# Optimization experiments

Measured on AMD Instinct MI355X. Metric: run time of the kernel, lower is better.

## Reference

```python
import jax, jax.numpy as jnp
import numpy as np

H = 4  # heads


def _tconv(x, src, dst, ea, Wq, bq, Wk, bk, Wv, bv, We, Ws, bs):
    # PyG TransformerConv, heads=4, concat=False, root_weight=True, beta=False
    N = x.shape[0]
    Dh = Wq.shape[1] // H  # per-head dim (= hidden_channels)
    q = (x @ Wq + bq).reshape(N, H, Dh)
    k = (x @ Wk + bk).reshape(N, H, Dh)
    v = (x @ Wv + bv).reshape(N, H, Dh)
    e = (ea @ We).reshape(-1, H, Dh)      # lin_edge has no bias in PyG
    kj = k[src] + e                        # [E, H, Dh]
    vj = v[src] + e                        # [E, H, Dh]
    alpha = (q[dst] * kj).sum(-1) / jnp.sqrt(jnp.asarray(Dh, x.dtype))  # [E, H]
    # segment softmax over incoming edges of each dst node
    m = jax.ops.segment_max(alpha, dst, num_segments=N)
    a = jnp.exp(alpha - m[dst])
    s = jax.ops.segment_sum(a, dst, num_segments=N)
    a = a / (s[dst] + 1e-16)
    out = jax.ops.segment_sum(a[:, :, None] * vj, dst, num_segments=N)  # [N, H, Dh]
    out = out.mean(axis=1)                 # concat=False -> mean over heads
    return out + x @ Ws + bs               # root/skip connection


def setup_inputs() -> dict:
    key = jax.random.key(0)
    ks = jax.random.split(key, 32)
    N, E, C_in, C_e, Ch = 50000, 800000, 32, 16, 32
    d = {}
    d['x'] = jax.random.normal(ks[0], (N, C_in), dtype=jnp.float32)
    d['edge_attr'] = jax.random.normal(ks[1], (E, C_e), dtype=jnp.float32)
    d['edge_index'] = jax.random.randint(ks[2], (2, E), 0, N, dtype=jnp.int32)
    s = 0.05
    i = 3
    for L, cin in ((1, C_in), (2, Ch)):
        d[f'Wq{L}'] = jax.random.normal(ks[i], (cin, H * Ch)) * s; i += 1
        d[f'bq{L}'] = jnp.zeros((H * Ch,), jnp.float32)
        d[f'Wk{L}'] = jax.random.normal(ks[i], (cin, H * Ch)) * s; i += 1
        d[f'bk{L}'] = jnp.zeros((H * Ch,), jnp.float32)
        d[f'Wv{L}'] = jax.random.normal(ks[i], (cin, H * Ch)) * s; i += 1
        d[f'bv{L}'] = jnp.zeros((H * Ch,), jnp.float32)
        d[f'We{L}'] = jax.random.normal(ks[i], (C_e, H * Ch)) * s; i += 1
        d[f'Ws{L}'] = jax.random.normal(ks[i], (cin, Ch)) * s; i += 1
        d[f'bs{L}'] = jnp.zeros((Ch,), jnp.float32)
    d['Wm1'] = jax.random.normal(ks[i], (2 * Ch + C_e, Ch)) * s; i += 1
    d['bm1'] = jnp.zeros((Ch,), jnp.float32)
    d['Wm2'] = jax.random.normal(ks[i], (Ch, 1)) * s; i += 1
    d['bm2'] = jnp.zeros((1,), jnp.float32)
    return d


def reference(x, edge_attr, edge_index,
              Wq1, bq1, Wk1, bk1, Wv1, bv1, We1, Ws1, bs1,
              Wq2, bq2, Wk2, bk2, Wv2, bv2, We2, Ws2, bs2,
              Wm1, bm1, Wm2, bm2):
    src, dst = edge_index[0], edge_index[1]
    h = jax.nn.relu(_tconv(x, src, dst, edge_attr, Wq1, bq1, Wk1, bk1, Wv1, bv1, We1, Ws1, bs1))
    h = jax.nn.relu(_tconv(h, src, dst, edge_attr, Wq2, bq2, Wk2, bk2, Wv2, bv2, We2, Ws2, bs2))
    ef = jnp.concatenate([h[src], edge_attr, h[dst]], axis=-1)  # [E, 2*Ch + C_e]
    out = jax.nn.relu(ef @ Wm1 + bm1) @ Wm2 + bm2
    return out.reshape(-1)
```

## Files before the change

kernel.cpp:

```cpp
#include <hip/hip_runtime.h>
#include <hip/hip_fp16.h>
#include <math.h>

#define D128 128
#define CH32 32
#define CE16 16

__global__ void k_hist(const int* __restrict__ dst, int* __restrict__ deg, int E) {
    int e = blockIdx.x * blockDim.x + threadIdx.x;
    if (e < E) atomicAdd(&deg[dst[e]], 1);
}

__global__ void k_scan1(const int* __restrict__ deg, int* __restrict__ offs,
                        int* __restrict__ bsum, int N) {
    __shared__ int buf[256];
    int t = threadIdx.x;
    int i = blockIdx.x * 256 + t;
    int v = (i < N) ? deg[i] : 0;
    buf[t] = v;
    __syncthreads();
    #pragma unroll
    for (int off = 1; off < 256; off <<= 1) {
        int val = (t >= off) ? buf[t - off] : 0;
        __syncthreads();
        buf[t] += val;
        __syncthreads();
    }
    if (i < N) offs[i] = buf[t] - v;
    if (t == 255) bsum[blockIdx.x] = buf[255];
}

__global__ void k_scan2(const int* __restrict__ bsum, int* __restrict__ boff, int nb) {
    __shared__ int buf[256];
    int t = threadIdx.x;
    int v = (t < nb) ? bsum[t] : 0;
    buf[t] = v;
    __syncthreads();
    #pragma unroll
    for (int off = 1; off < 256; off <<= 1) {
        int val = (t >= off) ? buf[t - off] : 0;
        __syncthreads();
        buf[t] += val;
        __syncthreads();
    }
    if (t < nb) boff[t] = buf[t] - v;
}

__global__ void k_scan3(const int* __restrict__ boff, int* __restrict__ offs,
                        int* __restrict__ cur, int N, int E) {
    int i = blockIdx.x * blockDim.x + threadIdx.x;
    if (i < N) {
        int o = offs[i] + boff[i >> 8];
        offs[i] = o;
        cur[i] = o;
    }
    if (i == 0) offs[N] = E;
}

__global__ void k_scatter(const int* __restrict__ src, const int* __restrict__ dst,
                          int* __restrict__ cur, int* __restrict__ csr_srcb,
                          float4* __restrict__ ea_csr4, const float4* __restrict__ ea4,
                          int E) {
    int e = blockIdx.x * blockDim.x + threadIdx.x;
    if (e < E) {
        int d = dst[e];
        int p = atomicAdd(&cur[d], 1);
        csr_srcb[p] = src[e] << 9;
        float4 a0 = ea4[e * 4 + 0];
        float4 a1 = ea4[e * 4 + 1];
        float4 a2 = ea4[e * 4 + 2];
        float4 a3 = ea4[e * 4 + 3];
        ea_csr4[p * 4 + 0] = a0;
        ea_csr4[p * 4 + 1] = a1;
        ea_csr4[p * 4 + 2] = a2;
        ea_csr4[p * 4 + 3] = a3;
    }
}

__global__ void k_wqe(const float* __restrict__ Wq, const float* __restrict__ bq,
                      const float* __restrict__ We,
                      float* __restrict__ Wqe, float* __restrict__ bqe) {
    int t = threadIdx.x;
    int h = t >> 4, j = t & 15;
    const float QS = 0.17677669529663687f * 1.4426950408889634f;
    float wecol[32];
    #pragma unroll
    for (int d = 0; d < 32; d++) wecol[d] = We[j * D128 + h * 32 + d];
    for (int i = 0; i < 32; i++) {
        float s = 0.f;
        #pragma unroll
        for (int d = 0; d < 32; d++) s = fmaf(Wq[i * D128 + h * 32 + d], wecol[d], s);
        Wqe[i * 64 + t] = s * QS;
    }
    float s = 0.f;
    #pragma unroll
    for (int d = 0; d < 32; d++) s = fmaf(bq[h * 32 + d], wecol[d], s);
    bqe[t] = s * QS;
}

__global__ __launch_bounds__(256) void k_qeproj(
    const float* __restrict__ x, const float* __restrict__ Wqe,
    const float* __restrict__ bqe, float* __restrict__ qeb, int N) {
    __shared__ float W[32][64];
    __shared__ float xs[4][32];
    int tid = threadIdx.x;
    for (int i = tid; i < 32 * 64; i += 256) W[i >> 6][i & 63] = Wqe[i];
    int col = tid & 63, r = tid >> 6;
    float b = bqe[col];
    __syncthreads();
    int nchunk = (N + 3) / 4;
    for (int chk = blockIdx.x; chk < nchunk; chk += gridDim.x) {
        int n = chk * 4 + r;
        if (tid < 128) {
            int rr = tid >> 5, cc = tid & 31;
            int nn = chk * 4 + rr;
            xs[rr][cc] = (nn < N) ? x[nn * 32 + cc] : 0.f;
        }
        __syncthreads();
        if (n < N) {
            float a = b;
            #pragma unroll
            for (int j = 0; j < 32; j++) a = fmaf(xs[r][j], W[j][col], a);
            qeb[(size_t)n * 64 + col] = a;
        }
        __syncthreads();
    }
}

__global__ __launch_bounds__(128) void k_nodeproj(
    const float* __restrict__ xin,
    const float* __restrict__ Wq, const float* __restrict__ bq,
    const float* __restrict__ Wk, const float* __restrict__ bk,
    const float* __restrict__ Wv, const float* __restrict__ bv,
    const float* __restrict__ Ws, const float* __restrict__ bs,
    float* __restrict__ q, __half* __restrict__ kvh,
    float* __restrict__ skip, int N)
{
    int tid = threadIdx.x;
    int c   = tid & 31;
    int pos = ((tid >> 2) << 3) | (tid & 3);
    float wq[32], wk[32], wv[32], ws[32];
    #pragma unroll
    for (int j = 0; j < 32; j++) {
        wq[j] = Wq[j * D128 + tid];
        wk[j] = Wk[j * D128 + tid];
        wv[j] = Wv[j * D128 + tid];
        ws[j] = Ws[j * CH32 + c];
    }
    float bqc = bq[tid], bkc = bk[tid], bvc = bv[tid], bsc = bs[c];
    __shared__ float xs[4][32];
    int nchunk = (N + 3) / 4;
    for (int chk = blockIdx.x; chk < nchunk; chk += gridDim.x) {
        int base = chk * 4;
        {
            int r = tid >> 5;
            int n = base + r;
            xs[r][c] = (n < N) ? xin[n * 32 + c] : 0.f;
        }
        __syncthreads();
        #pragma unroll
        for (int r = 0; r < 4; r++) {
            int n = base + r;
            if (n < N) {
                float aq = bqc, ak = bkc, av = bvc;
                #pragma unroll
                for (int j = 0; j < 32; j++) {
                    float xj = xs[r][j];
                    aq = fmaf(xj, wq[j], aq);
                    ak = fmaf(xj, wk[j], ak);
                    av = fmaf(xj, wv[j], av);
                }
                q[n * D128 + tid] = aq;
                kvh[(size_t)n * 256 + pos]     = __float2half_rn(ak);
                kvh[(size_t)n * 256 + pos + 4] = __float2half_rn(av);
            }
        }
        {
            int r = tid >> 5;
            int n = base + r;
            if (n < N) {
                float as = bsc;
                #pragma unroll
                for (int j = 0; j < 32; j++) as = fmaf(xs[r][j], ws[j], as);
                skip[n * 32 + c] = as;
            }
        }
        __syncthreads();
    }
}

__global__ __launch_bounds__(64) void k_edgeattn(
    const float* __restrict__ q, const __half* __restrict__ kvh,
    const float* __restrict__ skip,
    const float* __restrict__ ea_csr, const float* __restrict__ We,
    const int* __restrict__ offs, const int* __restrict__ csr_srcb,
    const float* __restrict__ qeb, float* __restrict__ hout)
{
    int node = blockIdx.x;
    int lane = threadIdx.x;
    int eg   = lane >> 5;
    int c    = lane & 31;
    int g    = c & 7;
    int c4   = c << 2;

    const float QS = 0.17677669529663687f * 1.4426950408889634f;
    float4 qv = *(const float4*)&q[(size_t)node * D128 + c4];
    qv.x *= QS; qv.y *= QS; qv.z *= QS; qv.w *= QS;

    float2 qe01 = *(const float2*)&qeb[(size_t)node * 64 + ((c >> 3) << 4) + 2 * g];
    float qe0 = qe01.x, qe1 = qe01.y;

    int s0 = offs[node], s1 = offs[node + 1];
    int deg = s1 - s0;

    float l = 0.f;
    float ac0 = 0.f, ac1 = 0.f, ac2 = 0.f, ac3 = 0.f;
    float se0 = 0.f, se1 = 0.f;

    if (deg > 0) {
        int last = s1 - 1;
        const char* kvb = (const char*)kvh;
        int toff = c << 4;

        auto eidx = [&](int p) { return min(s0 + 2 * p + eg, last); };
        auto ldidx = [&](int p) { return csr_srcb[eidx(p)]; };
        auto ldkv  = [&](int ib) {
            return *(const float4*)(kvb + (size_t)(unsigned)ib + toff);
        };
        auto ldea  = [&](int p) {
            return *(const float2*)&ea_csr[(size_t)eidx(p) * 16 + 2 * g];
        };
        auto pair = [&](const float4& kvr, const float2& eav, int p) {
            bool valid = (s0 + 2 * p + eg) <= last;
            float2 k01 = __half22float2(*(const __half2*)&kvr.x);
            float2 k23 = __half22float2(*(const __half2*)&kvr.y);
            float2 v01 = __half22float2(*(const __half2*)&kvr.z);
            float2 v23 = __half22float2(*(const __half2*)&kvr.w);
            float t = fmaf(qv.y, k01.y, qv.x * k01.x);
            t = fmaf(qv.z, k23.x, t);
            t = fmaf(qv.w, k23.y, t);
            t = fmaf(qe0, eav.x, t);
            t = fmaf(qe1, eav.y, t);
            t += __shfl_xor(t, 1);
            t += __shfl_xor(t, 2);
            t += __shfl_xor(t, 4);
            float pp = valid ? __builtin_amdgcn_exp2f(t) : 0.f;
            l += pp;
            ac0 = fmaf(pp, v01.x, ac0);
            ac1 = fmaf(pp, v01.y, ac1);
            ac2 = fmaf(pp, v23.x, ac2);
            ac3 = fmaf(pp, v23.y, ac3);
            se0 = fmaf(pp, eav.x, se0);
            se1 = fmaf(pp, eav.y, se1);
        };

        int iA0 = ldidx(0), iA1 = ldidx(1);
        int iB0 = ldidx(2), iB1 = ldidx(3);
        float4 kA0 = ldkv(iA0), kA1 = ldkv(iA1);
        float2 eA0 = ldea(0),   eA1 = ldea(1);

        int p = 0;
        int nIter = (deg + 7) >> 3;
        for (int it = 0; it < nIter; ++it) {
            float4 kB0 = ldkv(iB0), kB1 = ldkv(iB1);
            float2 eB0 = ldea(p + 2), eB1 = ldea(p + 3);
            iA0 = ldidx(p + 4); iA1 = ldidx(p + 5);

            pair(kA0, eA0, p + 0);
            pair(kA1, eA1, p + 1);

            kA0 = ldkv(iA0); kA1 = ldkv(iA1);
            eA0 = ldea(p + 4); eA1 = ldea(p + 5);
            iB0 = ldidx(p + 6); iB1 = ldidx(p + 7);

            pair(kB0, eB0, p + 2);
            pair(kB1, eB1, p + 3);

            p += 4;
        }
    }

    l   += __shfl_xor(l, 32);
    ac0 += __shfl_xor(ac0, 32);
    ac1 += __shfl_xor(ac1, 32);
    ac2 += __shfl_xor(ac2, 32);
    ac3 += __shfl_xor(ac3, 32);
    se0 += __shfl_xor(se0, 32);
    se1 += __shfl_xor(se1, 32);

    float inv = 1.0f / (l + 1e-16f);
    float r0 = ac0 * inv, r1 = ac1 * inv, r2 = ac2 * inv, r3 = ac3 * inv;
    float sn0 = se0 * inv, sn1 = se1 * inv;

    int gb = lane & ~7;
    #pragma unroll
    for (int j = 0; j < 16; j++) {
        float sj = __shfl((j & 1) ? sn1 : sn0, gb | (j >> 1), 64);
        float4 wj = *(const float4*)&We[j * D128 + c4];
        r0 = fmaf(sj, wj.x, r0);
        r1 = fmaf(sj, wj.y, r1);
        r2 = fmaf(sj, wj.z, r2);
        r3 = fmaf(sj, wj.w, r3);
    }
    r0 += __shfl_xor(r0, 8);  r0 += __shfl_xor(r0, 16);
    r1 += __shfl_xor(r1, 8);  r1 += __shfl_xor(r1, 16);
    r2 += __shfl_xor(r2, 8);  r2 += __shfl_xor(r2, 16);
    r3 += __shfl_xor(r3, 8);  r3 += __shfl_xor(r3, 16);
    if (lane < 8) {
        const float4 sk = *(const float4*)&skip[(size_t)node * 32 + c4];
        float4 o;
        o.x = fmaxf(fmaf(0.25f, r0, sk.x), 0.f);
        o.y = fmaxf(fmaf(0.25f, r1, sk.y), 0.f);
        o.z = fmaxf(fmaf(0.25f, r2, sk.z), 0.f);
        o.w = fmaxf(fmaf(0.25f, r3, sk.w), 0.f);
        *(float4*)&hout[(size_t)node * 32 + c4] = o;
    }
}

__global__ __launch_bounds__(256) void k_postproj(
    const float* __restrict__ h, const float* __restrict__ Wm1,
    const float* __restrict__ bm1, float* __restrict__ hA,
    float* __restrict__ hC, int N) {
    __shared__ float WA[32][32], WC[32][32];
    __shared__ float hs[8][32];
    int tid = threadIdx.x;
    for (int i = tid; i < 1024; i += 256) {
        WA[i >> 5][i & 31] = Wm1[i];
        WC[i >> 5][i & 31] = Wm1[48 * 32 + i];
    }
    int col = tid & 31, r = tid >> 5;
    float bb = bm1[col];
    __syncthreads();
    int nchunk = (N + 7) / 8;
    for (int chk = blockIdx.x; chk < nchunk; chk += gridDim.x) {
        int n = chk * 8 + r;
        hs[r][col] = (n < N) ? h[(size_t)n * 32 + col] : 0.f;
        __syncthreads();
        if (n < N) {
            float a = bb, cc = 0.f;
            #pragma unroll
            for (int j = 0; j < 32; j++) {
                float hj = hs[r][j];
                a  = fmaf(hj, WA[j][col], a);
                cc = fmaf(hj, WC[j][col], cc);
            }
            hA[(size_t)n * 32 + col] = a;
            hC[(size_t)n * 32 + col] = cc;
        }
        __syncthreads();
    }
}

__global__ __launch_bounds__(256) void k_mlp(
    const float* __restrict__ hA, const float* __restrict__ hC,
    const float* __restrict__ ea,
    const int* __restrict__ src, const int* __restrict__ dst,
    const float* __restrict__ Wm1, const float* __restrict__ Wm2,
    const float* __restrict__ bm2, float* __restrict__ out, int E)
{
    __shared__ float4 B4[16 * 8];
    __shared__ float wm2L[32];
    int tid = threadIdx.x;
    const float4* Wm1B = (const float4*)(Wm1 + 32 * 32);
    for (int i = tid; i < 128; i += 256) B4[i] = Wm1B[i];
    if (tid < 32) wm2L[tid] = Wm2[tid];
    __syncthreads();

    int e = blockIdx.x * 256 + tid;
    if (e >= E) return;
    float b2 = bm2[0];
    int s = src[e], d = dst[e];

    const float4* pa  = (const float4*)(hA + (size_t)s * 32);
    const float4* pc  = (const float4*)(hC + (size_t)d * 32);
    const float4* eav = (const float4*)(ea + (size_t)e * 16);

    float4 acc[8];
    #pragma unroll
    for (int i = 0; i < 8; i++) {
        float4 va = pa[i], vc = pc[i];
        acc[i] = make_float4(va.x + vc.x, va.y + vc.y, va.z + vc.z, va.w + vc.w);
    }

    auto dorow = [&](int j, float xj) {
        #pragma unroll
        for (int c4 = 0; c4 < 8; c4++) {
            float4 w = B4[j * 8 + c4];
            acc[c4].x = fmaf(xj, w.x, acc[c4].x);
            acc[c4].y = fmaf(xj, w.y, acc[c4].y);
            acc[c4].z = fmaf(xj, w.z, acc[c4].z);
            acc[c4].w = fmaf(xj, w.w, acc[c4].w);
        }
    };

    #pragma unroll
    for (int qd = 0; qd < 4; qd++) {
        float4 xv = eav[qd];
        dorow(qd * 4 + 0, xv.x); dorow(qd * 4 + 1, xv.y);
        dorow(qd * 4 + 2, xv.z); dorow(qd * 4 + 3, xv.w);
    }

    float y = b2;
    #pragma unroll
    for (int c4 = 0; c4 < 8; c4++) {
        y += fmaxf(acc[c4].x, 0.f) * wm2L[c4 * 4 + 0];
        y += fmaxf(acc[c4].y, 0.f) * wm2L[c4 * 4 + 1];
        y += fmaxf(acc[c4].z, 0.f) * wm2L[c4 * 4 + 2];
        y += fmaxf(acc[c4].w, 0.f) * wm2L[c4 * 4 + 3];
    }
    out[e] = y;
}

extern "C" void kernel_launch(void* const* d_in, const int* in_sizes, int n_in,
                              void* d_out, int out_size, void* d_ws, size_t ws_size,
                              hipStream_t stream)
{
    const float* x  = (const float*)d_in[0];
    const float* ea = (const float*)d_in[1];
    const int*   ei = (const int*)d_in[2];
    const int N = in_sizes[0] / 32;
    const int E = in_sizes[1] / 16;
    const int* src = ei;
    const int* dst = ei + E;

    const float *Wq1 = (const float*)d_in[3],  *bq1 = (const float*)d_in[4];
    const float *Wk1 = (const float*)d_in[5],  *bk1 = (const float*)d_in[6];
    const float *Wv1 = (const float*)d_in[7],  *bv1 = (const float*)d_in[8];
    const float *We1 = (const float*)d_in[9],  *Ws1 = (const float*)d_in[10];
    const float *bs1 = (const float*)d_in[11];
    const float *Wq2 = (const float*)d_in[12], *bq2 = (const float*)d_in[13];
    const float *Wk2 = (const float*)d_in[14], *bk2 = (const float*)d_in[15];
    const float *Wv2 = (const float*)d_in[16], *bv2 = (const float*)d_in[17];
    const float *We2 = (const float*)d_in[18], *Ws2 = (const float*)d_in[19];
    const float *bs2 = (const float*)d_in[20];
    const float *Wm1 = (const float*)d_in[21], *bm1 = (const float*)d_in[22];
    const float *Wm2 = (const float*)d_in[23], *bm2 = (const float*)d_in[24];

    char* w = (char*)d_ws;
    auto alloc = [&](size_t bytes) -> void* {
        void* p = (void*)w;
        w += (bytes + 255) & ~(size_t)255;
        return p;
    };
    int* deg      = (int*)alloc((size_t)N * 4);
    int* offs     = (int*)alloc(((size_t)N + 1) * 4);
    int* cur      = (int*)alloc((size_t)N * 4);
    int* bsum     = (int*)alloc(256 * 4);
    int* boff     = (int*)alloc(256 * 4);
    int* csr_srcb = (int*)alloc((size_t)E * 4);
    float* ea_csr = (float*)alloc((size_t)E * 16 * 4);
    float* qb     = (float*)alloc((size_t)N * 128 * 4);
    __half* kvb   = (__half*)alloc((size_t)N * 256 * 2);
    float* skipb  = (float*)alloc((size_t)N * 32 * 4);
    float* h1     = (float*)alloc((size_t)N * 32 * 4);
    float* h2     = (float*)alloc((size_t)N * 32 * 4);
    float* Wqe1   = (float*)alloc(32 * 64 * 4);
    float* bqe1   = (float*)alloc(64 * 4);
    float* Wqe2   = (float*)alloc(32 * 64 * 4);
    float* bqe2   = (float*)alloc(64 * 4);
    float* qeb    = (float*)alloc((size_t)N * 64 * 4);
    float* hA     = (float*)alloc((size_t)N * 32 * 4);
    float* hC     = (float*)alloc((size_t)N * 32 * 4);

    hipMemsetAsync(deg, 0, (size_t)N * 4, stream);

    int ebl = (E + 255) / 256;
    int nb  = (N + 255) / 256;
    k_hist<<<ebl, 256, 0, stream>>>(dst, deg, E);
    k_scan1<<<nb, 256, 0, stream>>>(deg, offs, bsum, N);
    k_scan2<<<1, 256, 0, stream>>>(bsum, boff, nb);
    k_scan3<<<nb, 256, 0, stream>>>(boff, offs, cur, N, E);
    k_scatter<<<ebl, 256, 0, stream>>>(src, dst, cur, csr_srcb,
                                       (float4*)ea_csr, (const float4*)ea, E);
    k_wqe<<<1, 64, 0, stream>>>(Wq1, bq1, We1, Wqe1, bqe1);
    k_wqe<<<1, 64, 0, stream>>>(Wq2, bq2, We2, Wqe2, bqe2);

    k_nodeproj<<<1024, 128, 0, stream>>>(x, Wq1, bq1, Wk1, bk1, Wv1, bv1, Ws1, bs1,
                                         qb, kvb, skipb, N);
    k_qeproj<<<1024, 256, 0, stream>>>(x, Wqe1, bqe1, qeb, N);
    k_edgeattn<<<N, 64, 0, stream>>>(qb, kvb, skipb, ea_csr, We1,
                                     offs, csr_srcb, qeb, h1);
    k_nodeproj<<<1024, 128, 0, stream>>>(h1, Wq2, bq2, Wk2, bk2, Wv2, bv2, Ws2, bs2,
                                         qb, kvb, skipb, N);
    k_qeproj<<<1024, 256, 0, stream>>>(h1, Wqe2, bqe2, qeb, N);
    k_edgeattn<<<N, 64, 0, stream>>>(qb, kvb, skipb, ea_csr, We2,
                                     offs, csr_srcb, qeb, h2);
    k_postproj<<<1024, 256, 0, stream>>>(h2, Wm1, bm1, hA, hC, N);
    k_mlp<<<ebl, 256, 0, stream>>>(hA, hC, ea, src, dst, Wm1, Wm2, bm2,
                                   (float*)d_out, E);
}
```

Before: 558.4 us.

## Fuse qe projection into nodeproj, parallelize wqe, run MLP in CSR order

The qe projection (x @ Wqe) moves into k_nodeproj, which reuses the shared x tile and removes a separate kernel that re-read node features. k_wqe runs as one 66-block launch covering both layers instead of two single-block launches. The edge MLP now walks edges in CSR (dst-sorted) order, so hC reads become sequential and edge_attr comes from the already-permuted buffer, then scatters results back through a stored edge id. The cost is two extra E-sized int arrays written during the scatter and non-coalesced output writes.

```diff
diff --git a/kernel.cpp b/kernel.cpp
--- a/kernel.cpp
+++ b/kernel.cpp
@@ -59,6 +59,7 @@
 
 __global__ void k_scatter(const int* __restrict__ src, const int* __restrict__ dst,
                           int* __restrict__ cur, int* __restrict__ csr_srcb,
+                          int* __restrict__ csr_dst, int* __restrict__ csr_eid,
                           float4* __restrict__ ea_csr4, const float4* __restrict__ ea4,
                           int E) {
     int e = blockIdx.x * blockDim.x + threadIdx.x;
@@ -66,6 +67,8 @@
         int d = dst[e];
         int p = atomicAdd(&cur[d], 1);
         csr_srcb[p] = src[e] << 9;
+        csr_dst[p] = d;
+        csr_eid[p] = e;
         float4 a0 = ea4[e * 4 + 0];
         float4 a1 = ea4[e * 4 + 1];
         float4 a2 = ea4[e * 4 + 2];
@@ -77,54 +80,30 @@
     }
 }
 
-__global__ void k_wqe(const float* __restrict__ Wq, const float* __restrict__ bq,
-                      const float* __restrict__ We,
-                      float* __restrict__ Wqe, float* __restrict__ bqe) {
-    int t = threadIdx.x;
-    int h = t >> 4, j = t & 15;
+__global__ void k_wqe(const float* __restrict__ Wq1, const float* __restrict__ bq1,
+                      const float* __restrict__ We1,
+                      const float* __restrict__ Wq2, const float* __restrict__ bq2,
+                      const float* __restrict__ We2,
+                      float* __restrict__ Wqe1, float* __restrict__ bqe1,
+                      float* __restrict__ Wqe2, float* __restrict__ bqe2) {
+    int t = threadIdx.x, h = t >> 4, j = t & 15;
     const float QS = 0.17677669529663687f * 1.4426950408889634f;
-    float wecol[32];
-    #pragma unroll
-    for (int d = 0; d < 32; d++) wecol[d] = We[j * D128 + h * 32 + d];
-    for (int i = 0; i < 32; i++) {
-        float s = 0.f;
-        #pragma unroll
-        for (int d = 0; d < 32; d++) s = fmaf(Wq[i * D128 + h * 32 + d], wecol[d], s);
-        Wqe[i * 64 + t] = s * QS;
-    }
+    int b = blockIdx.x;
+    int layer = (b >= 33);
+    int i = layer ? b - 33 : b;
+    const float* Wq = layer ? Wq2 : Wq1;
+    const float* bq = layer ? bq2 : bq1;
+    const float* We = layer ? We2 : We1;
+    float* Wqe = layer ? Wqe2 : Wqe1;
+    float* bqe = layer ? bqe2 : bqe1;
+    const float* base = (i < 32) ? (Wq + i * D128) : bq;
     float s = 0.f;
     #pragma unroll
-    for (int d = 0; d < 32; d++) s = fmaf(bq[h * 32 + d], wecol[d], s);
-    bqe[t] = s * QS;
-}
-
-__global__ __launch_bounds__(256) void k_qeproj(
-    const float* __restrict__ x, const float* __restrict__ Wqe,
-    const float* __restrict__ bqe, float* __restrict__ qeb, int N) {
-    __shared__ float W[32][64];
-    __shared__ float xs[4][32];
-    int tid = threadIdx.x;
-    for (int i = tid; i < 32 * 64; i += 256) W[i >> 6][i & 63] = Wqe[i];
-    int col = tid & 63, r = tid >> 6;
-    float b = bqe[col];
-    __syncthreads();
-    int nchunk = (N + 3) / 4;
-    for (int chk = blockIdx.x; chk < nchunk; chk += gridDim.x) {
-        int n = chk * 4 + r;
-        if (tid < 128) {
-            int rr = tid >> 5, cc = tid & 31;
-            int nn = chk * 4 + rr;
-            xs[rr][cc] = (nn < N) ? x[nn * 32 + cc] : 0.f;
-        }
-        __syncthreads();
-        if (n < N) {
-            float a = b;
-            #pragma unroll
-            for (int j = 0; j < 32; j++) a = fmaf(xs[r][j], W[j][col], a);
-            qeb[(size_t)n * 64 + col] = a;
-        }
-        __syncthreads();
-    }
+    for (int d = 0; d < 32; d++)
+        s = fmaf(base[h * 32 + d], We[j * D128 + h * 32 + d], s);
+    s *= QS;
+    if (i < 32) Wqe[i * 64 + t] = s;
+    else        bqe[t] = s;
 }
 
 __global__ __launch_bounds__(128) void k_nodeproj(
@@ -133,8 +112,9 @@
     const float* __restrict__ Wk, const float* __restrict__ bk,
     const float* __restrict__ Wv, const float* __restrict__ bv,
     const float* __restrict__ Ws, const float* __restrict__ bs,
+    const float* __restrict__ Wqe, const float* __restrict__ bqe,
     float* __restrict__ q, __half* __restrict__ kvh,
-    float* __restrict__ skip, int N)
+    float* __restrict__ skip, float* __restrict__ qeb, int N)
 {
     int tid = threadIdx.x;
     int c   = tid & 31;
@@ -148,7 +128,10 @@
         ws[j] = Ws[j * CH32 + c];
     }
     float bqc = bq[tid], bkc = bk[tid], bvc = bv[tid], bsc = bs[c];
+    __shared__ float wqeS[32][64];
     __shared__ float xs[4][32];
+    for (int i = tid; i < 2048; i += 128) wqeS[i >> 6][i & 63] = Wqe[i];
+    float bqec = bqe[tid & 63];
     int nchunk = (N + 3) / 4;
     for (int chk = blockIdx.x; chk < nchunk; chk += gridDim.x) {
         int base = chk * 4;
@@ -183,6 +166,21 @@
                 #pragma unroll
                 for (int j = 0; j < 32; j++) as = fmaf(xs[r][j], ws[j], as);
                 skip[n * 32 + c] = as;
+            }
+        }
+        {
+            int c6 = tid & 63;
+            int r0 = (tid >> 6) << 1;
+            #pragma unroll
+            for (int rr = 0; rr < 2; rr++) {
+                int n = base + r0 + rr;
+                if (n < N) {
+                    float a = bqec;
+                    #pragma unroll
+                    for (int j = 0; j < 32; j++)
+                        a = fmaf(xs[r0 + rr][j], wqeS[j][c6], a);
+                    qeb[(size_t)n * 64 + c6] = a;
+                }
             }
         }
         __syncthreads();
@@ -353,8 +351,9 @@
 
 __global__ __launch_bounds__(256) void k_mlp(
     const float* __restrict__ hA, const float* __restrict__ hC,
-    const float* __restrict__ ea,
-    const int* __restrict__ src, const int* __restrict__ dst,
+    const float* __restrict__ ea_csr,
+    const int* __restrict__ csr_srcb, const int* __restrict__ csr_dst,
+    const int* __restrict__ csr_eid,
     const float* __restrict__ Wm1, const float* __restrict__ Wm2,
     const float* __restrict__ bm2, float* __restrict__ out, int E)
 {
@@ -366,14 +365,16 @@
     if (tid < 32) wm2L[tid] = Wm2[tid];
     __syncthreads();
 
-    int e = blockIdx.x * 256 + tid;
-    if (e >= E) return;
+    int p = blockIdx.x * 256 + tid;
+    if (p >= E) return;
     float b2 = bm2[0];
-    int s = src[e], d = dst[e];
-
-    const float4* pa  = (const float4*)(hA + (size_t)s * 32);
+    int srcb = csr_srcb[p];
+    int d    = csr_dst[p];
+    int eid  = csr_eid[p];
+
+    const float4* pa  = (const float4*)((const char*)hA + ((size_t)(unsigned)srcb >> 2));
     const float4* pc  = (const float4*)(hC + (size_t)d * 32);
-    const float4* eav = (const float4*)(ea + (size_t)e * 16);
+    const float4* eav = (const float4*)(ea_csr + (size_t)p * 16);
 
     float4 acc[8];
     #pragma unroll
@@ -408,7 +409,7 @@
         y += fmaxf(acc[c4].z, 0.f) * wm2L[c4 * 4 + 2];
         y += fmaxf(acc[c4].w, 0.f) * wm2L[c4 * 4 + 3];
     }
-    out[e] = y;
+    out[eid] = y;
 }
 
 extern "C" void kernel_launch(void* const* d_in, const int* in_sizes, int n_in,
@@ -448,6 +449,8 @@
     int* bsum     = (int*)alloc(256 * 4);
     int* boff     = (int*)alloc(256 * 4);
     int* csr_srcb = (int*)alloc((size_t)E * 4);
+    int* csr_dst  = (int*)alloc((size_t)E * 4);
+    int* csr_eid  = (int*)alloc((size_t)E * 4);
     float* ea_csr = (float*)alloc((size_t)E * 16 * 4);
     float* qb     = (float*)alloc((size_t)N * 128 * 4);
     __half* kvb   = (__half*)alloc((size_t)N * 256 * 2);
@@ -466,26 +469,24 @@
 
     int ebl = (E + 255) / 256;
     int nb  = (N + 255) / 256;
+    k_wqe<<<66, 64, 0, stream>>>(Wq1, bq1, We1, Wq2, bq2, We2,
+                                 Wqe1, bqe1, Wqe2, bqe2);
     k_hist<<<ebl, 256, 0, stream>>>(dst, deg, E);
     k_scan1<<<nb, 256, 0, stream>>>(deg, offs, bsum, N);
     k_scan2<<<1, 256, 0, stream>>>(bsum, boff, nb);
     k_scan3<<<nb, 256, 0, stream>>>(boff, offs, cur, N, E);
-    k_scatter<<<ebl, 256, 0, stream>>>(src, dst, cur, csr_srcb,
+    k_scatter<<<ebl, 256, 0, stream>>>(src, dst, cur, csr_srcb, csr_dst, csr_eid,
                                        (float4*)ea_csr, (const float4*)ea, E);
-    k_wqe<<<1, 64, 0, stream>>>(Wq1, bq1, We1, Wqe1, bqe1);
-    k_wqe<<<1, 64, 0, stream>>>(Wq2, bq2, We2, Wqe2, bqe2);
 
     k_nodeproj<<<1024, 128, 0, stream>>>(x, Wq1, bq1, Wk1, bk1, Wv1, bv1, Ws1, bs1,
-                                         qb, kvb, skipb, N);
-    k_qeproj<<<1024, 256, 0, stream>>>(x, Wqe1, bqe1, qeb, N);
+                                         Wqe1, bqe1, qb, kvb, skipb, qeb, N);
     k_edgeattn<<<N, 64, 0, stream>>>(qb, kvb, skipb, ea_csr, We1,
                                      offs, csr_srcb, qeb, h1);
     k_nodeproj<<<1024, 128, 0, stream>>>(h1, Wq2, bq2, Wk2, bk2, Wv2, bv2, Ws2, bs2,
-                                         qb, kvb, skipb, N);
-    k_qeproj<<<1024, 256, 0, stream>>>(h1, Wqe2, bqe2, qeb, N);
+                                         Wqe2, bqe2, qb, kvb, skipb, qeb, N);
     k_edgeattn<<<N, 64, 0, stream>>>(qb, kvb, skipb, ea_csr, We2,
                                      offs, csr_srcb, qeb, h2);
     k_postproj<<<1024, 256, 0, stream>>>(h2, Wm1, bm1, hA, hC, N);
-    k_mlp<<<ebl, 256, 0, stream>>>(hA, hC, ea, src, dst, Wm1, Wm2, bm2,
-                                   (float*)d_out, E);
-}
+    k_mlp<<<ebl, 256, 0, stream>>>(hA, hC, ea_csr, csr_srcb, csr_dst, csr_eid,
+                                   Wm1, Wm2, bm2, (float*)d_out, E);
+}
```

Result: no change. 555.3 us (-0.6%).
